# Optimization experiments

Hardware: AMD Instinct MI355X
Metric: run time of the kernel (lower is better)

The kernel has to match this reference:

```python
import jax, jax.numpy as jnp
import numpy as np

NUM_HEADS = 8
LN_EPS = 1e-5


def _layernorm(x, g, b):
    m = jnp.mean(x, axis=-1, keepdims=True)
    v = jnp.mean(jnp.square(x - m), axis=-1, keepdims=True)
    return (x - m) * jax.lax.rsqrt(v + LN_EPS) * g + b


def setup_inputs() -> dict:
    key = jax.random.key(0)
    ks = jax.random.split(key, 10)
    D, C, Cin = 2, 256, 64  # depth, embed dim, input channels
    w = lambda k, shape: jax.random.normal(k, shape, jnp.float32) * 0.02
    return {
        "x": jax.random.normal(ks[0], (4, Cin, 12, 12, 12), jnp.float32),
        "W_pe": w(ks[1], (Cin, C)),
        "b_pe": jnp.zeros((C,), jnp.float32),
        "cls_token": w(ks[2], (1, 1, C)),
        "ln1_g": jnp.ones((D, C), jnp.float32),
        "ln1_b": jnp.zeros((D, C), jnp.float32),
        "Wqkv": w(ks[3], (D, C, 3 * C)),
        "Wproj": w(ks[4], (D, C, C)),
        "bproj": jnp.zeros((D, C), jnp.float32),
        "ln2_g": jnp.ones((D, C), jnp.float32),
        "ln2_b": jnp.zeros((D, C), jnp.float32),
        "W1": w(ks[5], (D, C, C)),
        "b1": jnp.zeros((D, C), jnp.float32),
        "W2": w(ks[6], (D, C, C)),
        "b2": jnp.zeros((D, C), jnp.float32),
        "normf_g": jnp.ones((C,), jnp.float32),
        "normf_b": jnp.zeros((C,), jnp.float32),
    }


def reference(x, W_pe, b_pe, cls_token, ln1_g, ln1_b, Wqkv, Wproj, bproj,
              ln2_g, ln2_b, W1, b1, W2, b2, normf_g, normf_b):
    B, Cin, H, W, L = x.shape
    C = W_pe.shape[1]
    hd = C // NUM_HEADS
    scale = hd ** (-0.5)

    # PatchEmbed: 1x1x1 Conv3d == per-voxel linear projection, then flatten to tokens
    tok = jnp.einsum('bchwl,cd->bhwld', x, W_pe).reshape(B, H * W * L, C) + b_pe
    cls = jnp.broadcast_to(cls_token, (B, 1, C))
    t = jnp.concatenate([cls, tok], axis=1)  # [B, N, C], N = H*W*L + 1
    N = t.shape[1]

    depth = Wqkv.shape[0]
    for i in range(depth):
        # --- self-attention ---
        y = _layernorm(t, ln1_g[i], ln1_b[i])
        qkv = (y @ Wqkv[i]).reshape(B, N, 3, NUM_HEADS, hd)
        qkv = jnp.transpose(qkv, (2, 0, 3, 1, 4))  # [3, B, H, N, hd]
        q, k, v = qkv[0], qkv[1], qkv[2]
        attn = jnp.einsum('bhnd,bhmd->bhnm', q, k) * scale
        attn = jax.nn.softmax(attn, axis=-1)
        o = jnp.einsum('bhnm,bhmd->bhnd', attn, v)
        o = jnp.transpose(o, (0, 2, 1, 3)).reshape(B, N, C)
        t = t + (o @ Wproj[i] + bproj[i])
        # --- MLP (mlp_ratio=1.0, exact GELU) ---
        y = _layernorm(t, ln2_g[i], ln2_b[i])
        h = jax.nn.gelu(y @ W1[i] + b1[i], approximate=False)
        t = t + (h @ W2[i] + b2[i])

    t = _layernorm(t, normf_g, normf_b)
    x_cls = t[:, 0]                                   # [B, C]
    feat = t[:, 1:]                                   # [B, H*W*L, C]
    feat = jnp.transpose(feat, (0, 2, 1)).reshape(B, C, H, W, L)  # downsample = Identity for dim=256
    return x_cls, feat
```

## Files before the change

### kernel.cpp

```cpp
#include <hip/hip_runtime.h>
#include <hip/hip_bf16.h>
#include <math.h>

#define B_   4
#define CIN  64
#define P_   1728
#define N_   1729
#define C_   256
#define NH_  8
#define HD_  32
#define M_   (B_*N_)
#define NPAD 1792

typedef __bf16 bf16x8 __attribute__((ext_vector_type(8)));
typedef __bf16 bf16x4 __attribute__((ext_vector_type(4)));
typedef float  f32x4  __attribute__((ext_vector_type(4)));

__global__ __launch_bounds__(256) void embed2(
    const float* __restrict__ x, const float* __restrict__ Wpe,
    const float* __restrict__ bpe, const float* __restrict__ cls,
    float* __restrict__ t)
{
    int idx = blockIdx.x*256 + threadIdx.x;
    int c   = idx & 255;
    int n   = (idx >> 8) % N_;
    int b   = idx / (N_*256);
    if (n == 0) { t[idx] = cls[c]; return; }
    int p = n - 1;
    float acc = bpe[c];
    for (int ci = 0; ci < CIN; ++ci)
        acc += x[(size_t)(b*CIN + ci)*P_ + p] * Wpe[ci*C_ + c];
    t[idx] = acc;
}

__global__ __launch_bounds__(256) void ln4(
    const float* __restrict__ in, __bf16* __restrict__ out,
    const float* __restrict__ g, const float* __restrict__ bb)
{
    int wv = threadIdx.x >> 6, lane = threadIdx.x & 63;
    size_t row = (size_t)blockIdx.x*4 + wv;
    float4 v = *(const float4*)&in[row*C_ + lane*4];
    float s1 = (v.x+v.y)+(v.z+v.w);
    float s2 = (v.x*v.x+v.y*v.y)+(v.z*v.z+v.w*v.w);
    #pragma unroll
    for (int off = 32; off >= 1; off >>= 1) {
        s1 += __shfl_xor(s1, off);
        s2 += __shfl_xor(s2, off);
    }
    float mean = s1*(1.0f/C_);
    float var  = fmaxf(s2*(1.0f/C_) - mean*mean, 0.0f);
    float rstd = rsqrtf(var + 1e-5f);
    float4 gg = *(const float4*)&g[lane*4];
    float4 bv = *(const float4*)&bb[lane*4];
    bf16x4 r;
    r[0] = (__bf16)((v.x-mean)*rstd*gg.x + bv.x);
    r[1] = (__bf16)((v.y-mean)*rstd*gg.y + bv.y);
    r[2] = (__bf16)((v.z-mean)*rstd*gg.z + bv.z);
    r[3] = (__bf16)((v.w-mean)*rstd*gg.w + bv.w);
    *(bf16x4*)&out[row*C_ + lane*4] = r;
}

__global__ __launch_bounds__(256) void ln4f(
    const float* __restrict__ in, float* __restrict__ out,
    const float* __restrict__ g, const float* __restrict__ bb,
    float* __restrict__ cls_out)
{
    int wv = threadIdx.x >> 6, lane = threadIdx.x & 63;
    size_t row = (size_t)blockIdx.x*4 + wv;
    float4 v = *(const float4*)&in[row*C_ + lane*4];
    float s1 = (v.x+v.y)+(v.z+v.w);
    float s2 = (v.x*v.x+v.y*v.y)+(v.z*v.z+v.w*v.w);
    #pragma unroll
    for (int off = 32; off >= 1; off >>= 1) {
        s1 += __shfl_xor(s1, off);
        s2 += __shfl_xor(s2, off);
    }
    float mean = s1*(1.0f/C_);
    float var  = fmaxf(s2*(1.0f/C_) - mean*mean, 0.0f);
    float rstd = rsqrtf(var + 1e-5f);
    float4 gg = *(const float4*)&g[lane*4];
    float4 bv = *(const float4*)&bb[lane*4];
    float4 r;
    r.x = (v.x-mean)*rstd*gg.x + bv.x;
    r.y = (v.y-mean)*rstd*gg.y + bv.y;
    r.z = (v.z-mean)*rstd*gg.z + bv.z;
    r.w = (v.w-mean)*rstd*gg.w + bv.w;
    *(float4*)&out[row*C_ + lane*4] = r;
    if ((row % N_) == 0)
        *(float4*)&cls_out[(row / N_)*C_ + lane*4] = r;
}

__global__ __launch_bounds__(256) void wprep2(
    const float* __restrict__ Wqkv, const float* __restrict__ Wproj,
    const float* __restrict__ W1,   const float* __restrict__ W2,
    __bf16* __restrict__ wT)
{
    int z = blockIdx.z, which = z >> 1, layer = z & 1;
    const float* src; __bf16* dst; int NC;
    if (which == 0) {
        src = Wqkv + (size_t)layer*C_*768;
        dst = wT   + (size_t)layer*768*256;
        NC  = 768;
    } else {
        NC = 256;
        const float* b3 = (which == 1) ? Wproj : (which == 2) ? W1 : W2;
        src = b3 + (size_t)layer*65536;
        dst = wT + 2*768*256 + (size_t)((which-1)*2 + layer)*65536;
    }
    int n0 = blockIdx.x*32; if (n0 >= NC) return;
    int k0 = blockIdx.y*32;
    __shared__ float tile[32][33];
    int c = threadIdx.x & 31, r = threadIdx.x >> 5;
    for (int rr = r; rr < 32; rr += 8)
        tile[rr][c] = src[(size_t)(k0+rr)*NC + n0 + c];
    __syncthreads();
    for (int rr = r; rr < 32; rr += 8)
        dst[(size_t)(n0+rr)*256 + k0 + c] = (__bf16)tile[c][rr];
}

template<int NC, bool ADD, bool GELU, bool BIAS, bool OUTBF>
__global__ __launch_bounds__(256) void gemm3(
    const __bf16* __restrict__ A, const __bf16* __restrict__ Wt,
    const float* __restrict__ bias, float* __restrict__ outF,
    __bf16* __restrict__ outB)
{
    __shared__ __align__(16) __bf16 As[64*64];
    __shared__ __align__(16) __bf16 Bs[64*64];
    int r0 = blockIdx.x*64, c0 = blockIdx.y*64;
    int tid = threadIdx.x;
    int wv = tid >> 6, lane = tid & 63, quad = lane >> 4, mn = lane & 15;
    int sr = tid >> 2, sc = tid & 3;
    int ga = r0 + sr; if (ga >= M_) ga = M_ - 1;

    f32x4 acc[4];
    #pragma unroll
    for (int ct = 0; ct < 4; ++ct)
        #pragma unroll
        for (int rr = 0; rr < 4; ++rr) acc[ct][rr] = 0.f;

    for (int kc = 0; kc < 4; ++kc) {
        __syncthreads();
        *(bf16x8*)&As[sr*64 + ((sc ^ (sr & 7))*8)] =
            *(const bf16x8*)&A[(size_t)ga*256 + kc*64 + sc*8];
        *(bf16x8*)&As[sr*64 + (((sc+4) ^ (sr & 7))*8)] =
            *(const bf16x8*)&A[(size_t)ga*256 + kc*64 + sc*8 + 32];
        *(bf16x8*)&Bs[sr*64 + ((sc ^ (sr & 7))*8)] =
            *(const bf16x8*)&Wt[(size_t)(c0+sr)*256 + kc*64 + sc*8];
        *(bf16x8*)&Bs[sr*64 + (((sc+4) ^ (sr & 7))*8)] =
            *(const bf16x8*)&Wt[(size_t)(c0+sr)*256 + kc*64 + sc*8 + 32];
        __syncthreads();

        #pragma unroll
        for (int h = 0; h < 2; ++h) {
            bf16x8 a = *(const bf16x8*)&As[(wv*16 + mn)*64 + (((h*4+quad) ^ (mn & 7))*8)];
            #pragma unroll
            for (int ct = 0; ct < 4; ++ct) {
                bf16x8 b = *(const bf16x8*)&Bs[(ct*16 + mn)*64 + (((h*4+quad) ^ (mn & 7))*8)];
                acc[ct] = __builtin_amdgcn_mfma_f32_16x16x32_bf16(a, b, acc[ct], 0, 0, 0);
            }
        }
    }

    #pragma unroll
    for (int ct = 0; ct < 4; ++ct) {
        int col = c0 + ct*16 + mn;
        #pragma unroll
        for (int rr = 0; rr < 4; ++rr) {
            int row = r0 + wv*16 + quad*4 + rr;
            if (row >= M_) continue;
            float val = acc[ct][rr];
            if (BIAS) val += bias[col];
            if (GELU) val = 0.5f*val*(1.f + erff(val*0.70710678118654752f));
            size_t oi = (size_t)row*NC + col;
            if (OUTBF) outB[oi] = (__bf16)val;
            else if (ADD) outF[oi] += val;
            else outF[oi] = val;
        }
    }
}

__global__ __launch_bounds__(256) void gemm_qkv3(
    const __bf16* __restrict__ A, const __bf16* __restrict__ Wt,
    __bf16* __restrict__ qB, __bf16* __restrict__ kB, __bf16* __restrict__ vB)
{
    __shared__ __align__(16) __bf16 As[64*64];
    __shared__ __align__(16) __bf16 Bs[64*64];
    int r0 = blockIdx.x*64, c0 = blockIdx.y*64;
    int tid = threadIdx.x;
    int wv = tid >> 6, lane = tid & 63, quad = lane >> 4, mn = lane & 15;
    int sr = tid >> 2, sc = tid & 3;
    int ga = r0 + sr; if (ga >= M_) ga = M_ - 1;

    f32x4 acc[4];
    #pragma unroll
    for (int ct = 0; ct < 4; ++ct)
        #pragma unroll
        for (int rr = 0; rr < 4; ++rr) acc[ct][rr] = 0.f;

    for (int kc = 0; kc < 4; ++kc) {
        __syncthreads();
        *(bf16x8*)&As[sr*64 + ((sc ^ (sr & 7))*8)] =
            *(const bf16x8*)&A[(size_t)ga*256 + kc*64 + sc*8];
        *(bf16x8*)&As[sr*64 + (((sc+4) ^ (sr & 7))*8)] =
            *(const bf16x8*)&A[(size_t)ga*256 + kc*64 + sc*8 + 32];
        *(bf16x8*)&Bs[sr*64 + ((sc ^ (sr & 7))*8)] =
            *(const bf16x8*)&Wt[(size_t)(c0+sr)*256 + kc*64 + sc*8];
        *(bf16x8*)&Bs[sr*64 + (((sc+4) ^ (sr & 7))*8)] =
            *(const bf16x8*)&Wt[(size_t)(c0+sr)*256 + kc*64 + sc*8 + 32];
        __syncthreads();

        #pragma unroll
        for (int h = 0; h < 2; ++h) {
            bf16x8 a = *(const bf16x8*)&As[(wv*16 + mn)*64 + (((h*4+quad) ^ (mn & 7))*8)];
            #pragma unroll
            for (int ct = 0; ct < 4; ++ct) {
                bf16x8 b = *(const bf16x8*)&Bs[(ct*16 + mn)*64 + (((h*4+quad) ^ (mn & 7))*8)];
                acc[ct] = __builtin_amdgcn_mfma_f32_16x16x32_bf16(a, b, acc[ct], 0, 0, 0);
            }
        }
    }

    const float scale = 0.17677669529663687f;
    #pragma unroll
    for (int ct = 0; ct < 4; ++ct) {
        int col = c0 + ct*16 + mn;
        #pragma unroll
        for (int rr = 0; rr < 4; ++rr) {
            int row = r0 + wv*16 + quad*4 + rr;
            if (row >= M_) continue;
            int b = row / N_, n = row - b*N_;
            float val = acc[ct][rr];
            if (col < 256) {
                int h = col >> 5, dd = col & 31;
                qB[((size_t)(b*NH_+h)*NPAD + n)*32 + dd] = (__bf16)(val*scale);
            } else if (col < 512) {
                int h = (col-256) >> 5, dd = col & 31;
                kB[((size_t)(b*NH_+h)*NPAD + n)*32 + dd] = (__bf16)val;
            } else {
                int h = (col-512) >> 5, dd = col & 31;
                vB[((size_t)(b*NH_+h)*32 + dd)*NPAD + n] = (__bf16)val;
            }
        }
    }
}

__global__ __launch_bounds__(256) void attn10(
    const __bf16* __restrict__ qB, const __bf16* __restrict__ kB,
    const __bf16* __restrict__ vB, __bf16* __restrict__ o)
{
    int bh = blockIdx.x, b = bh >> 3, h = bh & 7;
    int q0 = blockIdx.y * 64;
    int tid = threadIdx.x;
    int wv = tid >> 6, lane = tid & 63, quad = lane >> 4, mn = lane & 15;

    __shared__ __align__(16) __bf16 lk[128*32];
    __shared__ __align__(16) __bf16 lvt[32*128];
    __shared__ __align__(16) __bf16 lp[4][16*72];

    bf16x8 qfrag = *(const bf16x8*)(
        qB + ((size_t)bh*NPAD + q0 + wv*16 + mn)*32 + quad*8);

    bf16x8 vones;
    #pragma unroll
    for (int j = 0; j < 8; ++j) vones[j] = (mn == 0) ? (__bf16)1.0f : (__bf16)0.0f;

    f32x4 oacc0, oacc1, oacc2;
    #pragma unroll
    for (int rr = 0; rr < 4; ++rr) { oacc0[rr]=0.f; oacc1[rr]=0.f; oacc2[rr]=0.f; }

    const __bf16* kbase = kB + (size_t)bh*NPAD*32;
    const __bf16* vbase = vB + (size_t)bh*32*NPAD;
    int sr = tid >> 2, sc = tid & 3;
    int vr = tid >> 3, vc = tid & 7;

    for (int t = 0; t < 14; ++t) {
        int k0 = t*128;
        __syncthreads();
        #pragma unroll
        for (int hh = 0; hh < 2; ++hh) {
            int r = hh*64 + sr;
            *(bf16x8*)&lk[r*32 + ((sc ^ (r & 3))*8)] =
                *(const bf16x8*)(kbase + (size_t)(k0 + r)*32 + sc*8);
            int cp = hh*8 + vc;
            *(bf16x8*)&lvt[vr*128 + ((cp ^ (vr & 7))*8)] =
                *(const bf16x8*)(vbase + (size_t)vr*NPAD + k0 + cp*8);
        }
        __syncthreads();

        #pragma unroll
        for (int h2 = 0; h2 < 2; ++h2) {
            f32x4 s[4];
            #pragma unroll
            for (int ct = 0; ct < 4; ++ct) {
                int kr = h2*64 + ct*16 + mn;
                bf16x8 kf = *(const bf16x8*)&lk[kr*32 + ((quad ^ (mn & 3))*8)];
                f32x4 z;
                #pragma unroll
                for (int rr = 0; rr < 4; ++rr) z[rr] = 0.f;
                s[ct] = __builtin_amdgcn_mfma_f32_16x16x32_bf16(qfrag, kf, z, 0, 0, 0);
            }

            #pragma unroll
            for (int ct = 0; ct < 4; ++ct) {
                bool valid = (k0 + h2*64 + ct*16 + mn) < N_;
                #pragma unroll
                for (int rr = 0; rr < 4; ++rr) {
                    float p = valid ? __expf(s[ct][rr]) : 0.f;
                    lp[wv][(quad*4+rr)*72 + ct*16 + mn] = (__bf16)p;
                }
            }

            #pragma unroll
            for (int kh = 0; kh < 2; ++kh) {
                bf16x8 pf = *(const bf16x8*)&lp[wv][mn*72 + kh*32 + quad*8];
                int chunk = h2*8 + kh*4 + quad;
                int vsw = (chunk ^ (mn & 7)) * 8;
                bf16x8 v0 = *(const bf16x8*)&lvt[ mn      *128 + vsw];
                bf16x8 v1 = *(const bf16x8*)&lvt[(mn+16)*128 + vsw];
                oacc0 = __builtin_amdgcn_mfma_f32_16x16x32_bf16(pf, v0, oacc0, 0, 0, 0);
                oacc1 = __builtin_amdgcn_mfma_f32_16x16x32_bf16(pf, v1, oacc1, 0, 0, 0);
                oacc2 = __builtin_amdgcn_mfma_f32_16x16x32_bf16(pf, vones, oacc2, 0, 0, 0);
            }
        }
    }

    #pragma unroll
    for (int rr = 0; rr < 4; ++rr) {
        float l = __shfl(oacc2[rr], lane & 48);
        int q = q0 + wv*16 + quad*4 + rr;
        if (q >= N_) continue;
        float inv = 1.0f / l;
        size_t base = ((size_t)(b*N_ + q))*C_ + h*HD_;
        o[base + mn]      = (__bf16)(oacc0[rr]*inv);
        o[base + 16 + mn] = (__bf16)(oacc1[rr]*inv);
    }
}

__global__ __launch_bounds__(256) void feat3(
    const float* __restrict__ y, float* __restrict__ outf)
{
    __shared__ float tl[32][33];
    int p0 = blockIdx.x*32, c0 = blockIdx.y*32, b = blockIdx.z;
    int cc = threadIdx.x & 31, rr = threadIdx.x >> 5;
    for (int i = rr; i < 32; i += 8)
        tl[i][cc] = y[((size_t)(b*N_) + 1 + p0 + i)*C_ + c0 + cc];
    __syncthreads();
    for (int i = rr; i < 32; i += 8)
        outf[((size_t)(b*C_) + c0 + i)*P_ + p0 + cc] = tl[cc][i];
}

extern "C" void kernel_launch(void* const* d_in, const int* in_sizes, int n_in,
                              void* d_out, int out_size, void* d_ws, size_t ws_size,
                              hipStream_t stream)
{
    const float* x        = (const float*)d_in[0];
    const float* W_pe     = (const float*)d_in[1];
    const float* b_pe     = (const float*)d_in[2];
    const float* cls_tok  = (const float*)d_in[3];
    const float* ln1_g    = (const float*)d_in[4];
    const float* ln1_b    = (const float*)d_in[5];
    const float* Wqkv     = (const float*)d_in[6];
    const float* Wproj    = (const float*)d_in[7];
    const float* bproj    = (const float*)d_in[8];
    const float* ln2_g    = (const float*)d_in[9];
    const float* ln2_b    = (const float*)d_in[10];
    const float* W1       = (const float*)d_in[11];
    const float* b1       = (const float*)d_in[12];
    const float* W2       = (const float*)d_in[13];
    const float* b2       = (const float*)d_in[14];
    const float* normf_g  = (const float*)d_in[15];
    const float* normf_b  = (const float*)d_in[16];

    const size_t MC = (size_t)M_*C_;
    float*  ws  = (float*)d_ws;
    float*  t   = ws;
    float*  yf  = ws + MC;
    __bf16* ybf = (__bf16*)(ws + 2*MC);
    __bf16* hbf = (__bf16*)(ws + 2*MC + MC/2);
    __bf16* obf = (__bf16*)(ws + 2*MC + MC);
    __bf16* wT  = (__bf16*)(ws + 2*MC + 3*(MC/2));
    __bf16* qB  = wT + 2*768*256 + 6*256*256;
    __bf16* kB  = qB + (size_t)B_*NH_*NPAD*32;
    __bf16* vB  = kB + (size_t)B_*NH_*NPAD*32;

    __bf16* projT = wT + 2*768*256;
    __bf16* w1T   = projT + 2*256*256;
    __bf16* w2T   = w1T   + 2*256*256;

    float* out_cls  = (float*)d_out;
    float* out_feat = out_cls + B_*C_;

    wprep2<<<dim3(24, 8, 8), 256, 0, stream>>>(Wqkv, Wproj, W1, W2, wT);
    embed2<<<(B_*N_*C_)/256, 256, 0, stream>>>(x, W_pe, b_pe, cls_tok, t);

    const int GRID_M = (M_ + 63) / 64;
    for (int i = 0; i < 2; ++i) {
        ln4<<<M_/4, 256, 0, stream>>>(t, ybf, ln1_g + i*C_, ln1_b + i*C_);
        gemm_qkv3<<<dim3(GRID_M, 12), 256, 0, stream>>>(
            ybf, wT + (size_t)i*768*256, qB, kB, vB);
        attn10<<<dim3(32, 28), 256, 0, stream>>>(qB, kB, vB, obf);
        gemm3<256,true,false,true,false><<<dim3(GRID_M, 4), 256, 0, stream>>>(
            obf, projT + (size_t)i*65536, bproj + i*C_, t, nullptr);
        ln4<<<M_/4, 256, 0, stream>>>(t, ybf, ln2_g + i*C_, ln2_b + i*C_);
        gemm3<256,false,true,true,true><<<dim3(GRID_M, 4), 256, 0, stream>>>(
            ybf, w1T + (size_t)i*65536, b1 + i*C_, nullptr, hbf);
        gemm3<256,true,false,true,false><<<dim3(GRID_M, 4), 256, 0, stream>>>(
            hbf, w2T + (size_t)i*65536, b2 + i*C_, t, nullptr);
    }

    ln4f<<<M_/4, 256, 0, stream>>>(t, yf, normf_g, normf_b, out_cls);
    feat3<<<dim3(54, 8, 4), 256, 0, stream>>>(yf, out_feat);
}
```

Measured before the change: 303.4 us.

## Zero-pad K/V tails and drop masking and ones-MFMA row sum in attention

Adds a kernel that zeroes the padded key/value rows beyond N, so the attention kernel can skip the per-element validity mask. Padded keys then give exp(0)=1, and a constant 63 is subtracted from the row sum to compensate. The softmax denominator is accumulated in registers with shuffles, replacing a third MFMA against a ones vector. The QK product is computed transposed so each lane writes P to shared memory as one packed 4-element store. The scheme relies on the constant padding count and on the pad rows staying zero across layers.

After: 293.4 us. -3.3%, faster.

```diff
diff --git a/kernel.cpp b/kernel.cpp
--- a/kernel.cpp
+++ b/kernel.cpp
@@ -116,6 +116,18 @@
     __syncthreads();
     for (int rr = r; rr < 32; rr += 8)
         dst[(size_t)(n0+rr)*256 + k0 + c] = (__bf16)tile[c][rr];
+}
+
+__global__ __launch_bounds__(256) void padzero(
+    __bf16* __restrict__ kB, __bf16* __restrict__ vB)
+{
+    int idx = blockIdx.x*256 + threadIdx.x;
+    if (idx >= 32*63*32) return;
+    int d  = idx & 31;
+    int n  = (idx >> 5) % 63 + N_;
+    int bh = idx / (63*32);
+    kB[((size_t)bh*NPAD + n)*32 + d] = (__bf16)0.f;
+    vB[((size_t)bh*32 + d)*NPAD + n] = (__bf16)0.f;
 }
 
 template<int NC, bool ADD, bool GELU, bool BIAS, bool OUTBF>
@@ -244,7 +256,7 @@
     }
 }
 
-__global__ __launch_bounds__(256) void attn10(
+__global__ __launch_bounds__(256) void attn11(
     const __bf16* __restrict__ qB, const __bf16* __restrict__ kB,
     const __bf16* __restrict__ vB, __bf16* __restrict__ o)
 {
@@ -260,13 +272,10 @@
     bf16x8 qfrag = *(const bf16x8*)(
         qB + ((size_t)bh*NPAD + q0 + wv*16 + mn)*32 + quad*8);
 
-    bf16x8 vones;
-    #pragma unroll
-    for (int j = 0; j < 8; ++j) vones[j] = (mn == 0) ? (__bf16)1.0f : (__bf16)0.0f;
-
-    f32x4 oacc0, oacc1, oacc2;
-    #pragma unroll
-    for (int rr = 0; rr < 4; ++rr) { oacc0[rr]=0.f; oacc1[rr]=0.f; oacc2[rr]=0.f; }
+    f32x4 oacc0, oacc1;
+    #pragma unroll
+    for (int rr = 0; rr < 4; ++rr) { oacc0[rr]=0.f; oacc1[rr]=0.f; }
+    float lsum = 0.f;
 
     const __bf16* kbase = kB + (size_t)bh*NPAD*32;
     const __bf16* vbase = vB + (size_t)bh*32*NPAD;
@@ -289,7 +298,6 @@
 
         #pragma unroll
         for (int h2 = 0; h2 < 2; ++h2) {
-            f32x4 s[4];
             #pragma unroll
             for (int ct = 0; ct < 4; ++ct) {
                 int kr = h2*64 + ct*16 + mn;
@@ -297,17 +305,16 @@
                 f32x4 z;
                 #pragma unroll
                 for (int rr = 0; rr < 4; ++rr) z[rr] = 0.f;
-                s[ct] = __builtin_amdgcn_mfma_f32_16x16x32_bf16(qfrag, kf, z, 0, 0, 0);
-            }
-
-            #pragma unroll
-            for (int ct = 0; ct < 4; ++ct) {
-                bool valid = (k0 + h2*64 + ct*16 + mn) < N_;
+                f32x4 st = __builtin_amdgcn_mfma_f32_16x16x32_bf16(kf, qfrag, z, 0, 0, 0);
+
+                bf16x4 pf4;
                 #pragma unroll
                 for (int rr = 0; rr < 4; ++rr) {
-                    float p = valid ? __expf(s[ct][rr]) : 0.f;
-                    lp[wv][(quad*4+rr)*72 + ct*16 + mn] = (__bf16)p;
+                    float p = __expf(st[rr]);
+                    pf4[rr] = (__bf16)p;
+                    lsum += p;
                 }
+                *(bf16x4*)&lp[wv][mn*72 + ct*16 + quad*4] = pf4;
             }
 
             #pragma unroll
@@ -319,14 +326,17 @@
                 bf16x8 v1 = *(const bf16x8*)&lvt[(mn+16)*128 + vsw];
                 oacc0 = __builtin_amdgcn_mfma_f32_16x16x32_bf16(pf, v0, oacc0, 0, 0, 0);
                 oacc1 = __builtin_amdgcn_mfma_f32_16x16x32_bf16(pf, v1, oacc1, 0, 0, 0);
-                oacc2 = __builtin_amdgcn_mfma_f32_16x16x32_bf16(pf, vones, oacc2, 0, 0, 0);
             }
         }
     }
 
+    lsum += __shfl_xor(lsum, 16);
+    lsum += __shfl_xor(lsum, 32);
+    lsum -= 63.0f;
+
     #pragma unroll
     for (int rr = 0; rr < 4; ++rr) {
-        float l = __shfl(oacc2[rr], lane & 48);
+        float l = __shfl(lsum, quad*4 + rr);
         int q = q0 + wv*16 + quad*4 + rr;
         if (q >= N_) continue;
         float inv = 1.0f / l;
@@ -391,6 +401,7 @@
     float* out_feat = out_cls + B_*C_;
 
     wprep2<<<dim3(24, 8, 8), 256, 0, stream>>>(Wqkv, Wproj, W1, W2, wT);
+    padzero<<<252, 256, 0, stream>>>(kB, vB);
     embed2<<<(B_*N_*C_)/256, 256, 0, stream>>>(x, W_pe, b_pe, cls_tok, t);
 
     const int GRID_M = (M_ + 63) / 64;
@@ -398,7 +409,7 @@
         ln4<<<M_/4, 256, 0, stream>>>(t, ybf, ln1_g + i*C_, ln1_b + i*C_);
         gemm_qkv3<<<dim3(GRID_M, 12), 256, 0, stream>>>(
             ybf, wT + (size_t)i*768*256, qB, kB, vB);
-        attn10<<<dim3(32, 28), 256, 0, stream>>>(qB, kB, vB, obf);
+        attn11<<<dim3(32, 28), 256, 0, stream>>>(qB, kB, vB, obf);
         gemm3<256,true,false,true,false><<<dim3(GRID_M, 4), 256, 0, stream>>>(
             obf, projT + (size_t)i*65536, bproj + i*C_, t, nullptr);
         ln4<<<M_/4, 256, 0, stream>>>(t, ybf, ln2_g + i*C_, ln2_b + i*C_);
```
